# Kernel tuning notes

Measured on AMD Instinct MI355X. Metric: run time of the kernel, lower is better.

Reference implementation:

```python
import jax, jax.numpy as jnp
import numpy as np

B, S, HS = 2, 2048, 4096
NH, NKV = 32, 32
HD = HS // NH
INTER = 11008
VOCAB = 32000
EPS = 1e-6
ROPE_BASE = 10000.0


def setup_inputs() -> dict:
    key = jax.random.key(0)
    ks = jax.random.split(key, 16)
    sc = 0.02
    return {
        "hidden_states": jax.random.normal(ks[0], (B, S, HS), jnp.float32),
        "input_ids": jax.random.randint(ks[1], (B, S), 0, VOCAB, jnp.int32),
        "position_ids": jnp.arange(S, dtype=jnp.int32)[None, :],
        "embed": jax.random.normal(ks[2], (VOCAB, HS), jnp.float32) * sc,
        "fc_w": jax.random.normal(ks[3], (HS, 2 * HS), jnp.float32) * sc,
        "fc_b": jnp.zeros((HS,), jnp.float32),
        "q_w": jax.random.normal(ks[4], (NH * HD, HS), jnp.float32) * sc,
        "k_w": jax.random.normal(ks[5], (NKV * HD, HS), jnp.float32) * sc,
        "v_w": jax.random.normal(ks[6], (NKV * HD, HS), jnp.float32) * sc,
        "o_w": jax.random.normal(ks[7], (HS, NH * HD), jnp.float32) * sc,
        "gate_w": jax.random.normal(ks[8], (INTER, HS), jnp.float32) * sc,
        "up_w": jax.random.normal(ks[9], (INTER, HS), jnp.float32) * sc,
        "down_w": jax.random.normal(ks[10], (HS, INTER), jnp.float32) * sc,
        "post_ln_w": jnp.ones((HS,), jnp.float32),
    }


def _rotate_half(x):
    x1, x2 = jnp.split(x, 2, axis=-1)
    return jnp.concatenate((-x2, x1), axis=-1)


def _rms_norm(x, w, eps=EPS):
    x32 = x.astype(jnp.float32)
    x32 = x32 * jax.lax.rsqrt(jnp.mean(x32 * x32, axis=-1, keepdims=True) + eps)
    return (w * x32).astype(x.dtype)


def _forward(hidden_states, input_ids, position_ids, embed, fc_w, fc_b,
             q_w, k_w, v_w, o_w, gate_w, up_w, down_w, post_ln_w):
    # Embedding lookup (detached in original via no_grad)
    embeds = jax.lax.stop_gradient(embed[input_ids])  # [B,S,HS]
    h = jnp.concatenate((embeds, hidden_states), axis=-1) @ fc_w.T + fc_b  # [B,S,HS]

    # --- decoder layer 0 (no input_layernorm) ---
    residual = h
    q = (h @ q_w.T).reshape(B, S, NH, HD).transpose(0, 2, 1, 3)   # [B,NH,S,HD]
    k = (h @ k_w.T).reshape(B, S, NKV, HD).transpose(0, 2, 1, 3)
    v = (h @ v_w.T).reshape(B, S, NKV, HD).transpose(0, 2, 1, 3)

    # RoPE
    pos = position_ids[0].astype(jnp.float32)                      # [S]
    inv_freq = 1.0 / (ROPE_BASE ** (jnp.arange(0, HD, 2, dtype=jnp.float32) / HD))
    freqs = pos[:, None] * inv_freq[None, :]                       # [S,HD/2]
    emb = jnp.concatenate((freqs, freqs), axis=-1)                 # [S,HD]
    cos = jnp.cos(emb)[None, None, :, :]
    sin = jnp.sin(emb)[None, None, :, :]
    q = q * cos + _rotate_half(q) * sin
    k = k * cos + _rotate_half(k) * sin

    # attention (num_kv_groups == 1 here)
    scores = jnp.einsum('bhqd,bhkd->bhqk', q, k) / np.sqrt(HD)     # [B,NH,S,S]
    causal = jnp.triu(jnp.ones((S, S), bool), 1)
    scores = jnp.where(causal[None, None], -jnp.inf, scores)
    attn = jax.nn.softmax(scores.astype(jnp.float32), axis=-1).astype(q.dtype)
    out = jnp.einsum('bhqk,bhkd->bhqd', attn, v)                   # [B,NH,S,HD]
    out = out.transpose(0, 2, 1, 3).reshape(B, S, HS)
    attn_out = out @ o_w.T

    h = residual + attn_out
    residual = h
    hn = _rms_norm(h, post_ln_w)
    mlp = (jax.nn.silu(hn @ gate_w.T) * (hn @ up_w.T)) @ down_w.T
    return residual + mlp


def reference(hidden_states, input_ids, position_ids, embed, fc_w, fc_b,
              q_w, k_w, v_w, o_w, gate_w, up_w, down_w, post_ln_w):
    return _forward(hidden_states, input_ids, position_ids, embed, fc_w, fc_b,
                    q_w, k_w, v_w, o_w, gate_w, up_w, down_w, post_ln_w)
```

## Files before the change

### kernel.cpp

```cpp
#include <hip/hip_runtime.h>
#include <hip/hip_bf16.h>

typedef __attribute__((ext_vector_type(8))) short short8;
typedef __attribute__((ext_vector_type(4))) short short4v;
typedef __attribute__((ext_vector_type(4))) float floatx4;

#define B_SZ 2
#define S_SZ 2048
#define HS_SZ 4096
#define NH_SZ 32
#define HD_SZ 128
#define INTER_SZ 11008
#define M_TOT 4096
#define QKV_N 12288
#define GU_N 22016

__device__ __forceinline__ float b2f(short s){
  unsigned int u = ((unsigned int)(unsigned short)s) << 16;
  return __builtin_bit_cast(float, u);
}
__device__ __forceinline__ short f2b(float f){
  unsigned int u = __builtin_bit_cast(unsigned int, f);
  u = (u + 0x7FFFu + ((u >> 16) & 1u)) >> 16;
  return (short)u;
}

typedef __attribute__((address_space(1))) const unsigned int gu32;
typedef __attribute__((address_space(3))) unsigned int lu32;
__device__ __forceinline__ void gl2lds16(const short* g, short* l){
  __builtin_amdgcn_global_load_lds((gu32*)g, (lu32*)l, 16, 0, 0);
}

#define BARRIER() asm volatile("s_barrier" ::: "memory")
#define WAITV8()  asm volatile("s_waitcnt vmcnt(8)" ::: "memory")
#define WAITV4()  asm volatile("s_waitcnt vmcnt(4)" ::: "memory")
#define WAITV2()  asm volatile("s_waitcnt vmcnt(2)" ::: "memory")
#define WAITV0()  asm volatile("s_waitcnt vmcnt(0)" ::: "memory")

__global__ void cvt_bf16_kernel(const float* __restrict__ src, short* __restrict__ dst, long n8){
  long idx = (long)blockIdx.x * blockDim.x + threadIdx.x;
  if (idx >= n8) return;
  long e = idx * 8;
  floatx4 v0 = *(const floatx4*)(src + e);
  floatx4 v1 = *(const floatx4*)(src + e + 4);
  short8 o;
  o[0]=f2b(v0[0]); o[1]=f2b(v0[1]); o[2]=f2b(v0[2]); o[3]=f2b(v0[3]);
  o[4]=f2b(v1[0]); o[5]=f2b(v1[1]); o[6]=f2b(v1[2]); o[7]=f2b(v1[3]);
  *(short8*)(dst + e) = o;
}

__global__ void embed_concat_kernel(const float* __restrict__ hidden,
                                    const int* __restrict__ ids,
                                    const float* __restrict__ embed,
                                    short* __restrict__ X0){
  long idx = (long)blockIdx.x * blockDim.x + threadIdx.x;
  const long total = (long)M_TOT * (2*HS_SZ) / 4;
  if (idx >= total) return;
  long e = idx * 4;
  int m = (int)(e / (2*HS_SZ));
  int c = (int)(e % (2*HS_SZ));
  const float* src;
  if (c < HS_SZ){
    src = embed + (long)ids[m]*HS_SZ + c;
  } else {
    src = hidden + (long)m*HS_SZ + (c - HS_SZ);
  }
  floatx4 v = *(const floatx4*)src;
  short4v o;
  o[0]=f2b(v[0]); o[1]=f2b(v[1]); o[2]=f2b(v[2]); o[3]=f2b(v[3]);
  *(short4v*)(X0 + e) = o;
}

#define G_STAGE(op,h,kof,qb) { \
  gl2lds16(gs[op][h] + (kof), lds + (qb) + (op)*16384 + (h)*8192 + wid*1024); \
  gl2lds16(gs[op][h] + k8o[op] + (kof), lds + (qb) + (op)*16384 + (h)*8192 + wid*1024 + 512); }

#define LD_A(Mh,pb) { \
  _Pragma("unroll") \
  for (int mf=0; mf<4; mf++) \
    _Pragma("unroll") \
    for (int ks=0; ks<2; ks++) \
      af[mf][ks] = *(const short8*)(lds + (pb) + ((Mh)*128 + wr2*64 + mf*16 + lr)*64 + (((ks*4+lk)^lr7))*8); }

#define LD_B(BB,Nh,pb) { \
  _Pragma("unroll") \
  for (int nf=0; nf<2; nf++) \
    _Pragma("unroll") \
    for (int ks=0; ks<2; ks++) \
      BB[nf][ks] = *(const short8*)(lds + (pb) + 16384 + ((Nh)*128 + wc2*32 + nf*16 + lr)*64 + (((ks*4+lk)^lr7))*8); }

#define MMQ(Mh,Nh,BB) { \
  __builtin_amdgcn_s_setprio(1); \
  _Pragma("unroll") \
  for (int mf=0; mf<4; mf++) \
    _Pragma("unroll") \
    for (int nf=0; nf<2; nf++){ \
      acc[Mh][Nh][mf][nf] = __builtin_amdgcn_mfma_f32_16x16x32_bf16(af[mf][0], BB[nf][0], acc[Mh][Nh][mf][nf], 0,0,0); \
      acc[Mh][Nh][mf][nf] = __builtin_amdgcn_mfma_f32_16x16x32_bf16(af[mf][1], BB[nf][1], acc[Mh][Nh][mf][nf], 0,0,0); \
    } \
  __builtin_amdgcn_s_setprio(0); }

template<int EPI>
__global__ __launch_bounds__(512, 2)
void gemm256_kernel(const short* __restrict__ A, const short* __restrict__ Bw,
                    const short* __restrict__ Bw2, int nsplit,
                    int K, int lda, int ldc,
                    const float* __restrict__ bias,
                    const float* __restrict__ resid,
                    short* __restrict__ Cbf,
                    float* __restrict__ Cf){
  __shared__ __align__(16) short lds[65536];
  const int tid = threadIdx.x;
  const int wid = tid >> 6;
  const int lane = tid & 63;
  const int wr2 = wid >> 2, wc2 = wid & 3;
  const int lr = lane & 15, lk = lane >> 4;
  const int lr7 = lr & 7;

  const int nwg = gridDim.x * gridDim.y;
  const int id  = blockIdx.y * gridDim.x + blockIdx.x;
  const int cpx = nwg >> 3;
  const int sw  = (id & 7) * cpx + (id >> 3);
  const int bx  = sw % gridDim.x;
  const int by  = sw / gridDim.x;
  const int m0 = bx * 256, n0 = by * 256;

  const int srow = lane >> 3;
  const int sslot = (lane & 7) ^ srow;
  const long k8o[2] = { 8L * lda, 8L * K };
  const short* gs[2][2];
  #pragma unroll
  for (int h=0; h<2; h++){
    const int rowa = m0 + h*128 + wid*16 + srow;
    gs[0][h] = A + (long)rowa*lda + sslot*8;
    const int rowb = n0 + h*128 + wid*16 + srow;
    gs[1][h] = (rowb < nsplit ? Bw + (long)rowb*K
                              : Bw2 + (long)(rowb - nsplit)*K) + sslot*8;
  }

  floatx4 acc[2][2][4][2] = {};
  short8 af[4][2], b0[2][2], b1[2][2];
  const int nt = K >> 6;

  G_STAGE(0,0,0,0); G_STAGE(1,0,0,0); G_STAGE(1,1,0,0); G_STAGE(0,1,0,0);
  WAITV4(); BARRIER();

  for (int t = 0; t < nt-1; ++t){
    const int pb = (t & 1) << 15;
    const int qb = pb ^ 32768;
    const long kof = (long)(t+1) * 64;
    LD_A(0,pb); LD_B(b0,0,pb);
    G_STAGE(0,0,kof,qb);
    BARRIER();
    MMQ(0,0,b0);
    WAITV4(); BARRIER();
    LD_B(b1,1,pb);
    G_STAGE(1,0,kof,qb);
    BARRIER();
    MMQ(0,1,b1);
    WAITV4(); BARRIER();
    LD_A(1,pb);
    G_STAGE(1,1,kof,qb);
    BARRIER();
    MMQ(1,1,b1);
    BARRIER();
    G_STAGE(0,1,kof,qb);
    BARRIER();
    MMQ(1,0,b0);
    WAITV4(); BARRIER();
  }
  {
    const int pb = ((nt-1) & 1) << 15;
    LD_A(0,pb); LD_B(b0,0,pb);
    BARRIER(); MMQ(0,0,b0);
    WAITV2(); BARRIER();
    LD_B(b1,1,pb);
    BARRIER(); MMQ(0,1,b1);
    WAITV0(); BARRIER();
    LD_A(1,pb);
    BARRIER(); MMQ(1,1,b1);
    BARRIER();
    MMQ(1,0,b0);
  }

  #pragma unroll
  for (int Mh=0; Mh<2; Mh++){
    #pragma unroll
    for (int Nh=0; Nh<2; Nh++){
      #pragma unroll
      for (int mf=0; mf<4; mf++){
        #pragma unroll
        for (int nf=0; nf<2; nf++){
          const int col = n0 + Nh*128 + wc2*32 + nf*16 + lr;
          float bcol = (EPI==1) ? bias[col] : 0.0f;
          #pragma unroll
          for (int r=0; r<4; r++){
            const int row = m0 + Mh*128 + wr2*64 + mf*16 + lk*4 + r;
            float v = acc[Mh][Nh][mf][nf][r] + bcol;
            if (EPI==2) v += resid[(long)row*ldc + col];
            if (EPI==0 || EPI==1) Cbf[(long)row*ldc + col] = f2b(v);
            if (EPI==1 || EPI==2) Cf[(long)row*ldc + col] = v;
          }
        }
      }
    }
  }
}

__global__ void rope_kernel(short* __restrict__ qkv, const int* __restrict__ pos_ids){
  long idx = (long)blockIdx.x * blockDim.x + threadIdx.x;
  const long total = (long)M_TOT * NH_SZ * (HD_SZ/2);
  if (idx >= total) return;
  int i  = (int)(idx & 63);
  long rh = idx >> 6;
  int h  = (int)(rh & 31);
  int m  = (int)(rh >> 5);
  int s  = m & (S_SZ - 1);
  float p = (float)pos_ids[s];
  const float L2_10000 = 13.28771237954945f;
  float inv = exp2f(-(2.0f*i/(float)HD_SZ) * L2_10000);
  float fr = p * inv;
  float sn, cs;
  sincosf(fr, &sn, &cs);
  short* qp = qkv + (long)m*QKV_N + h*HD_SZ;
  short* kp = qp + HS_SZ;
  float q1=b2f(qp[i]), q2=b2f(qp[i+64]);
  qp[i]    = f2b(q1*cs - q2*sn);
  qp[i+64] = f2b(q2*cs + q1*sn);
  float k1=b2f(kp[i]), k2=b2f(kp[i+64]);
  kp[i]    = f2b(k1*cs - k2*sn);
  kp[i+64] = f2b(k2*cs + k1*sn);
}

__global__ __launch_bounds__(256)
void vtrans_kernel(const short* __restrict__ QKV, short* __restrict__ VT){
  __shared__ short tile[64][68];
  const int s0 = blockIdx.x * 64;
  const int d0 = blockIdx.y * 64;
  const int bh = blockIdx.z;
  const int b = bh >> 5, h = bh & 31;
  const int tid = threadIdx.x;
  #pragma unroll
  for (int it=0; it<2; it++){
    int e = (it*256 + tid) * 8;
    int ss = e >> 6, col = e & 63;
    short8 v = *(const short8*)(QKV + ((long)(b*S_SZ + s0 + ss))*QKV_N + 2*HS_SZ + h*HD_SZ + d0 + col);
    #pragma unroll
    for (int j=0;j<8;j++) tile[ss][col+j] = v[j];
  }
  __syncthreads();
  #pragma unroll
  for (int it=0; it<2; it++){
    int e = (it*256 + tid) * 8;
    int dd = e >> 6, scol = e & 63;
    short8 w;
    #pragma unroll
    for (int j=0;j<8;j++) w[j] = tile[scol+j][dd];
    *(short8*)(VT + ((long)(bh*HD_SZ + d0 + dd))*S_SZ + s0 + scol) = w;
  }
}

__global__ __launch_bounds__(256,2)
void attn_kernel(const short* __restrict__ QKV, const short* __restrict__ VT,
                 short* __restrict__ O){
  constexpr int LPD = 72;
  __shared__ __align__(16) short lds[32768];
  __shared__ __align__(16) short p_lds[4][16*LPD];
  const int bh = blockIdx.y;
  const int b = bh >> 5, h = bh & 31;
  const int q0 = blockIdx.x * 64;
  const int tid = threadIdx.x, wid = tid>>6, lane = tid&63;
  const int lr = lane & 15, lk = lane >> 4;
  const float scale = 0.08838834764831845f;

  const short* qbase = QKV + ((long)(b*S_SZ + q0 + wid*16))*QKV_N + h*HD_SZ;
  short8 qf[4];
  #pragma unroll
  for (int t=0;t<4;t++)
    qf[t] = *(const short8*)(qbase + (long)lr*QKV_N + t*32 + lk*8);

  const short* kb[4]; const short* vb[4];
  int kloff[4], vloff[4];
  #pragma unroll
  for (int p=0;p<4;p++){
    const int seg = wid*4 + p;
    const int rowk = seg*4 + (lane >> 4);
    const int slotk = (lane & 15) ^ (rowk & 15);
    kb[p] = QKV + ((long)(b*S_SZ) + rowk)*QKV_N + HS_SZ + h*HD_SZ + slotk*8;
    kloff[p] = seg*512;
    const int dv = seg*8 + (lane >> 3);
    const int slotv = (lane & 7) ^ (dv & 7);
    vb[p] = VT + ((long)(bh*HD_SZ + dv))*S_SZ + slotv*8;
    vloff[p] = 8192 + seg*512;
  }

  floatx4 oacc[8] = {};
  float m_run[4] = {-1e30f,-1e30f,-1e30f,-1e30f};
  float l_run[4] = {0.f,0.f,0.f,0.f};

  const int nt = blockIdx.x + 1;

  #pragma unroll
  for (int p=0;p<4;p++){
    gl2lds16(kb[p], lds + kloff[p]);
    gl2lds16(vb[p], lds + vloff[p]);
  }

  for (int t=0; t<nt; ++t){
    const int dbase = (t & 1) * 16384;
    const int nbase = ((t+1) & 1) * 16384;
    if (t+1 < nt){
      const long kkn = (long)(t+1)*64*QKV_N;
      const long vkn = (long)(t+1)*64;
      #pragma unroll
      for (int p=0;p<4;p++){
        gl2lds16(kb[p] + kkn, lds + nbase + kloff[p]);
        gl2lds16(vb[p] + vkn, lds + nbase + vloff[p]);
      }
      WAITV8();
    } else {
      WAITV0();
    }
    BARRIER();
    const int kv0 = t*64;
    floatx4 sfr[4];
    #pragma unroll
    for (int fn=0; fn<4; fn++){
      floatx4 s = {0.f,0.f,0.f,0.f};
      const int row = fn*16 + lr;
      #pragma unroll
      for (int tq=0; tq<4; tq++){
        short8 kf = *(const short8*)(lds + dbase + row*128 + (((tq*4+lk)^lr)&15)*8);
        s = __builtin_amdgcn_mfma_f32_16x16x32_bf16(qf[tq], kf, s, 0,0,0);
      }
      sfr[fn] = s;
    }
    float pv[4][4];
    #pragma unroll
    for (int fn=0; fn<4; fn++){
      const int col = kv0 + fn*16 + lr;
      #pragma unroll
      for (int r=0;r<4;r++){
        const int row = q0 + wid*16 + lk*4 + r;
        float sv = sfr[fn][r] * scale;
        pv[fn][r] = (col > row) ? -1e30f : sv;
      }
    }
    float mr4[4];
    int small = 1;
    #pragma unroll
    for (int r=0;r<4;r++){
      float mr = fmaxf(fmaxf(pv[0][r], pv[1][r]), fmaxf(pv[2][r], pv[3][r]));
      mr = fmaxf(mr, __shfl_xor(mr, 1, 16));
      mr = fmaxf(mr, __shfl_xor(mr, 2, 16));
      mr = fmaxf(mr, __shfl_xor(mr, 4, 16));
      mr = fmaxf(mr, __shfl_xor(mr, 8, 16));
      mr4[r] = mr;
      small &= (mr <= m_run[r] + 8.0f) ? 1 : 0;
    }
    const int skip = __all(small);
    float alpha_[4];
    #pragma unroll
    for (int r=0;r<4;r++){
      float mnew = skip ? m_run[r] : fmaxf(m_run[r], mr4[r]);
      alpha_[r] = skip ? 1.0f : __expf(m_run[r] - mnew);
      m_run[r] = mnew;
      float rs = 0.f;
      #pragma unroll
      for (int fn=0; fn<4; fn++){
        float e = __expf(pv[fn][r] - mnew);
        p_lds[wid][(lk*4+r)*LPD + fn*16 + lr] = f2b(e);
        rs += e;
      }
      rs += __shfl_xor(rs, 1, 16);
      rs += __shfl_xor(rs, 2, 16);
      rs += __shfl_xor(rs, 4, 16);
      rs += __shfl_xor(rs, 8, 16);
      l_run[r] = l_run[r]*alpha_[r] + rs;
    }
    if (!skip){
      #pragma unroll
      for (int f=0; f<8; f++){
        #pragma unroll
        for (int r=0;r<4;r++) oacc[f][r] *= alpha_[r];
      }
    }
    short8 pf[2];
    #pragma unroll
    for (int tp=0; tp<2; tp++)
      pf[tp] = *(const short8*)(&p_lds[wid][lr*LPD + tp*32 + lk*8]);
    #pragma unroll
    for (int f=0; f<8; f++){
      const int vrow = f*16 + lr;
      #pragma unroll
      for (int tp=0; tp<2; tp++){
        short8 vf = *(const short8*)(lds + dbase + 8192 + vrow*64 + (((tp*4+lk)^(lr&7))&7)*8);
        oacc[f] = __builtin_amdgcn_mfma_f32_16x16x32_bf16(pf[tp], vf, oacc[f], 0,0,0);
      }
    }
    BARRIER();
  }
  #pragma unroll
  for (int r=0;r<4;r++){
    const float inv = 1.0f / l_run[r];
    const long row = (long)(b*S_SZ + q0 + wid*16 + lk*4 + r);
    #pragma unroll
    for (int f=0; f<8; f++){
      O[row*HS_SZ + h*HD_SZ + f*16 + lr] = f2b(oacc[f][r]*inv);
    }
  }
}

__global__ void rmsnorm_kernel(const float* __restrict__ X, const float* __restrict__ W,
                               short* __restrict__ Y){
  const int row = blockIdx.x;
  const float* x = X + (long)row*HS_SZ;
  float ss = 0.f;
  for (int c = threadIdx.x*4; c < HS_SZ; c += 256*4){
    floatx4 v = *(const floatx4*)(x + c);
    ss += v[0]*v[0] + v[1]*v[1] + v[2]*v[2] + v[3]*v[3];
  }
  ss += __shfl_xor(ss, 32); ss += __shfl_xor(ss, 16);
  ss += __shfl_xor(ss, 8);  ss += __shfl_xor(ss, 4);
  ss += __shfl_xor(ss, 2);  ss += __shfl_xor(ss, 1);
  __shared__ float red[4];
  if ((threadIdx.x & 63) == 0) red[threadIdx.x >> 6] = ss;
  __syncthreads();
  ss = red[0] + red[1] + red[2] + red[3];
  const float rs = rsqrtf(ss / (float)HS_SZ + 1e-6f);
  for (int c = threadIdx.x*4; c < HS_SZ; c += 256*4){
    floatx4 v = *(const floatx4*)(x + c);
    floatx4 w = *(const floatx4*)(W + c);
    short4v o;
    o[0]=f2b(v[0]*rs*w[0]); o[1]=f2b(v[1]*rs*w[1]);
    o[2]=f2b(v[2]*rs*w[2]); o[3]=f2b(v[3]*rs*w[3]);
    *(short4v*)(Y + (long)row*HS_SZ + c) = o;
  }
}

__global__ void silu_mul_kernel(short* __restrict__ GU){
  long idx = (long)blockIdx.x * blockDim.x + threadIdx.x;
  const long total = (long)M_TOT * INTER_SZ / 8;
  if (idx >= total) return;
  long e = idx * 8;
  int m = (int)(e / INTER_SZ);
  int i = (int)(e - (long)m*INTER_SZ);
  long gix = (long)m*GU_N + i;
  short8 g = *(short8*)(GU + gix);
  short8 u = *(const short8*)(GU + gix + INTER_SZ);
  short8 o;
  #pragma unroll
  for (int j=0;j<8;j++){
    float gf = b2f(g[j]);
    float uf = b2f(u[j]);
    float s = gf / (1.0f + __expf(-gf));
    o[j] = f2b(s * uf);
  }
  *(short8*)(GU + gix) = o;
}

extern "C" void kernel_launch(void* const* d_in, const int* in_sizes, int n_in,
                              void* d_out, int out_size, void* d_ws, size_t ws_size,
                              hipStream_t stream){
  (void)in_sizes; (void)n_in; (void)out_size;
  const float* hidden = (const float*)d_in[0];
  const int*   ids    = (const int*)d_in[1];
  const int*   pos    = (const int*)d_in[2];
  const float* embed  = (const float*)d_in[3];
  const float* fc_w   = (const float*)d_in[4];
  const float* fc_b   = (const float*)d_in[5];
  const float* q_w    = (const float*)d_in[6];
  const float* k_w    = (const float*)d_in[7];
  const float* v_w    = (const float*)d_in[8];
  const float* o_w    = (const float*)d_in[9];
  const float* gate_w = (const float*)d_in[10];
  const float* up_w   = (const float*)d_in[11];
  const float* down_w = (const float*)d_in[12];
  const float* ln_w   = (const float*)d_in[13];

  char* ws = (char*)d_ws;
  size_t off = 0;
  auto alloc = [&](size_t bytes)->char*{
    char* p = ws + off;
    off = (off + bytes + 255) & ~(size_t)255;
    return p;
  };
  short* wbf   = (short*)alloc((size_t)INTER_SZ*HS_SZ*2);
  short* X0    = (short*)alloc((size_t)M_TOT*2*HS_SZ*2);
  short* h_bf  = (short*)alloc((size_t)M_TOT*HS_SZ*2);
  float* h_f   = (float*)alloc((size_t)M_TOT*HS_SZ*4);
  short* qkv_bf= (short*)alloc((size_t)M_TOT*QKV_N*2);
  short* vt_bf = (short*)alloc((size_t)M_TOT*HS_SZ*2);
  short* a_bf  = (short*)alloc((size_t)M_TOT*HS_SZ*2);
  float* h2_f  = (float*)alloc((size_t)M_TOT*HS_SZ*4);
  short* hn_bf = (short*)alloc((size_t)M_TOT*HS_SZ*2);
  short* gu_bf = (short*)alloc((size_t)M_TOT*GU_N*2);
  if (ws_size < off) return;

  short* wqkv   = gu_bf;
  short* wgate  = X0;

  auto cvt = [&](const float* src, short* dst, long n){
    long n8 = n / 8;
    cvt_bf16_kernel<<<(int)((n8 + 255)/256), 256, 0, stream>>>(src, dst, n8);
  };

  embed_concat_kernel<<<32768, 256, 0, stream>>>(hidden, ids, embed, X0);

  cvt(fc_w, wbf, (long)HS_SZ*2*HS_SZ);
  gemm256_kernel<1><<<dim3(16,16), 512, 0, stream>>>(X0, wbf, nullptr, 1<<30,
                                                     2*HS_SZ, 2*HS_SZ, HS_SZ,
                                                     fc_b, nullptr, h_bf, h_f);
  cvt(q_w, wqkv,                       (long)HS_SZ*HS_SZ);
  cvt(k_w, wqkv + (long)HS_SZ*HS_SZ,   (long)HS_SZ*HS_SZ);
  cvt(v_w, wqkv + 2L*HS_SZ*HS_SZ,      (long)HS_SZ*HS_SZ);
  gemm256_kernel<0><<<dim3(16,48), 512, 0, stream>>>(h_bf, wqkv, nullptr, 1<<30,
                                                     HS_SZ, HS_SZ, QKV_N,
                                                     nullptr, nullptr, qkv_bf, nullptr);
  rope_kernel<<<32768, 256, 0, stream>>>(qkv_bf, pos);
  vtrans_kernel<<<dim3(S_SZ/64, HD_SZ/64, B_SZ*NH_SZ), 256, 0, stream>>>(qkv_bf, vt_bf);
  attn_kernel<<<dim3(S_SZ/64, B_SZ*NH_SZ), 256, 0, stream>>>(qkv_bf, vt_bf, a_bf);
  cvt(o_w, wbf, (long)HS_SZ*HS_SZ);
  gemm256_kernel<2><<<dim3(16,16), 512, 0, stream>>>(a_bf, wbf, nullptr, 1<<30,
                                                     HS_SZ, HS_SZ, HS_SZ,
                                                     nullptr, h_f, nullptr, h2_f);
  rmsnorm_kernel<<<M_TOT, 256, 0, stream>>>(h2_f, ln_w, hn_bf);
  cvt(gate_w, wgate, (long)INTER_SZ*HS_SZ);
  cvt(up_w,   wbf,   (long)INTER_SZ*HS_SZ);
  gemm256_kernel<0><<<dim3(16,86), 512, 0, stream>>>(hn_bf, wgate, wbf, INTER_SZ,
                                                     HS_SZ, HS_SZ, GU_N,
                                                     nullptr, nullptr, gu_bf, nullptr);
  silu_mul_kernel<<<22016, 256, 0, stream>>>(gu_bf);
  cvt(down_w, wbf, (long)HS_SZ*INTER_SZ);
  gemm256_kernel<2><<<dim3(16,16), 512, 0, stream>>>(gu_bf, wbf, nullptr, 1<<30,
                                                     INTER_SZ, GU_N, HS_SZ,
                                                     nullptr, h2_f, nullptr, (float*)d_out);
}
```

Before: 2.294 ms.

## Deepen GEMM global-to-LDS prefetch to two K-tiles ahead

```diff
diff --git a/kernel.cpp b/kernel.cpp
--- a/kernel.cpp
+++ b/kernel.cpp
@@ -33,8 +33,6 @@
 
 #define BARRIER() asm volatile("s_barrier" ::: "memory")
 #define WAITV8()  asm volatile("s_waitcnt vmcnt(8)" ::: "memory")
-#define WAITV4()  asm volatile("s_waitcnt vmcnt(4)" ::: "memory")
-#define WAITV2()  asm volatile("s_waitcnt vmcnt(2)" ::: "memory")
 #define WAITV0()  asm volatile("s_waitcnt vmcnt(0)" ::: "memory")
 
 __global__ void cvt_bf16_kernel(const float* __restrict__ src, short* __restrict__ dst, long n8){
@@ -143,44 +141,39 @@
   const int nt = K >> 6;
 
   G_STAGE(0,0,0,0); G_STAGE(1,0,0,0); G_STAGE(1,1,0,0); G_STAGE(0,1,0,0);
-  WAITV4(); BARRIER();
-
-  for (int t = 0; t < nt-1; ++t){
+  if (nt > 1){
+    G_STAGE(0,0,64,32768); G_STAGE(1,0,64,32768);
+    G_STAGE(1,1,64,32768); G_STAGE(0,1,64,32768);
+    WAITV8();
+  } else {
+    WAITV0();
+  }
+  BARRIER();
+
+  for (int t = 0; t < nt; ++t){
     const int pb = (t & 1) << 15;
-    const int qb = pb ^ 32768;
-    const long kof = (long)(t+1) * 64;
+    const bool s2 = (t + 2 < nt);
+    const long kof2 = (long)(t+2) * 64;
     LD_A(0,pb); LD_B(b0,0,pb);
-    G_STAGE(0,0,kof,qb);
     BARRIER();
     MMQ(0,0,b0);
-    WAITV4(); BARRIER();
+    BARRIER();
     LD_B(b1,1,pb);
-    G_STAGE(1,0,kof,qb);
+    if (s2){ G_STAGE(0,0,kof2,pb); G_STAGE(1,0,kof2,pb); }
     BARRIER();
     MMQ(0,1,b1);
-    WAITV4(); BARRIER();
+    BARRIER();
     LD_A(1,pb);
-    G_STAGE(1,1,kof,qb);
+    if (s2) G_STAGE(1,1,kof2,pb);
     BARRIER();
     MMQ(1,1,b1);
     BARRIER();
-    G_STAGE(0,1,kof,qb);
+    if (s2) G_STAGE(0,1,kof2,pb);
     BARRIER();
     MMQ(1,0,b0);
-    WAITV4(); BARRIER();
-  }
-  {
-    const int pb = ((nt-1) & 1) << 15;
-    LD_A(0,pb); LD_B(b0,0,pb);
-    BARRIER(); MMQ(0,0,b0);
-    WAITV2(); BARRIER();
-    LD_B(b1,1,pb);
-    BARRIER(); MMQ(0,1,b1);
-    WAITV0(); BARRIER();
-    LD_A(1,pb);
-    BARRIER(); MMQ(1,1,b1);
-    BARRIER();
-    MMQ(1,0,b0);
+    if (s2) { WAITV8(); }
+    else if (t + 1 < nt) { WAITV0(); }
+    BARRIER();
   }
 
   #pragma unroll
```

Result: slower. 2.413 ms (+5.2%).
